# Kernel optimization log

Hardware: AMD Instinct MI355X
Metric: run time of the kernel (lower is better)

Reference implementation:

```python
import jax, jax.numpy as jnp
import numpy as np

B, M, L, H, V, HOPS = 32, 128, 32, 512, 32000, 3
NEG_INF = -1e9


def setup_inputs() -> dict:
    key = jax.random.key(0)
    k1, k2, k3, k4 = jax.random.split(key, 4)
    inputs = jax.random.randint(k1, (B, M, L), 0, V)          # memory token ids
    lengths = jax.random.randint(k2, (B, M), 1, L + 1)        # >0 so no all-masked rows
    enc_hidden = jax.random.normal(k3, (B, H), dtype=jnp.float32)
    # hop+1 embedding tables, normal_(0, 0.1) as in the torch init
    C = jax.random.normal(k4, (HOPS + 1, V, H), dtype=jnp.float32) * 0.1
    return {"inputs": inputs, "lengths": lengths, "enc_hidden": enc_hidden, "C": C}


def reference(inputs, lengths, enc_hidden, C):
    mask = lengths == 0                                       # [B, M] True -> masked

    def pool(table):
        # embedding gather [B,M,L,H] then sum over tokens -> [B,M,H]
        return table[inputs].sum(axis=2)

    u = enc_hidden                                            # [B, H]
    attns = []
    for h in range(HOPS):
        m_A = pool(C[h])                                      # [B, M, H]
        scores = jnp.einsum('bh,bmh->bm', u, m_A)             # dot attention
        scores = jnp.where(mask, NEG_INF, scores)
        attn = jax.nn.softmax(scores, axis=-1)                # [B, M]
        m_C = pool(C[h + 1])                                  # [B, M, H]
        u = u + jnp.einsum('bm,bmh->bh', attn, m_C)           # o_k combine
        attns.append(attn[:, None, :])                        # [B, 1, M] as in torch
    return u, jnp.stack(attns)                                # u_k [B,H], attns [HOPS,B,1,M]
```

## Files before the change

### kernel.cpp

```cpp
#include <hip/hip_runtime.h>

#define NB 32
#define NM 128
#define NL 32
#define NH 512
#define NV 32000
#define NHOPS 3
#define NEG_INF -1e9f

template <int NT>
__global__ __launch_bounds__(128)
void pool_kernel(const int* __restrict__ inputs,
                 const float* __restrict__ Ctab,
                 float* __restrict__ P) {
    const int bm  = blockIdx.x;
    const int tid = threadIdx.x;
    __shared__ int idx[NL];
    if (tid < NL) idx[tid] = inputs[bm * NL + tid];
    __syncthreads();

    const int hoff = tid * 4;
    float4 acc[NT];
#pragma unroll
    for (int t = 0; t < NT; ++t) acc[t] = make_float4(0.f, 0.f, 0.f, 0.f);

    for (int l = 0; l < NL; ++l) {
        const size_t rowbase = (size_t)idx[l] * NH + hoff;
#pragma unroll
        for (int t = 0; t < NT; ++t) {
            const float4 v = *reinterpret_cast<const float4*>(
                Ctab + (size_t)t * NV * NH + rowbase);
            acc[t].x += v.x; acc[t].y += v.y; acc[t].z += v.z; acc[t].w += v.w;
        }
    }
#pragma unroll
    for (int t = 0; t < NT; ++t) {
        *reinterpret_cast<float4*>(
            P + ((size_t)t * NB * NM + bm) * NH + hoff) = acc[t];
    }
}

__global__ __launch_bounds__(512)
void hop_kernel(const float* __restrict__ u_in,
                const float* __restrict__ PA,
                const float* __restrict__ PC,
                const int*   __restrict__ lengths,
                float* __restrict__ u_out,
                float* __restrict__ attn_out) {
    const int b   = blockIdx.x;
    const int tid = threadIdx.x;
    __shared__ float u_s[NH];
    __shared__ float sc[NM];
    __shared__ float tmp[512];

    u_s[tid] = u_in[b * NH + tid];
    __syncthreads();

    const int wave = tid >> 6;
    const int lane = tid & 63;
    for (int m = wave; m < NM; m += 8) {
        const float* row = PA + ((size_t)b * NM + m) * NH;
        float p = 0.f;
#pragma unroll
        for (int k = 0; k < NH / 64; ++k) {
            const int h = lane + k * 64;
            p += u_s[h] * row[h];
        }
#pragma unroll
        for (int off = 32; off; off >>= 1) p += __shfl_down(p, off, 64);
        if (lane == 0) sc[m] = p;
    }
    __syncthreads();

    float s = NEG_INF;
    if (tid < NM) s = (lengths[b * NM + tid] == 0) ? NEG_INF : sc[tid];
    tmp[tid] = s;
    __syncthreads();
    for (int st = 256; st >= 1; st >>= 1) {
        if (tid < st) tmp[tid] = fmaxf(tmp[tid], tmp[tid + st]);
        __syncthreads();
    }
    const float mx = tmp[0];
    __syncthreads();
    const float e = (tid < NM) ? expf(s - mx) : 0.f;
    tmp[tid] = e;
    __syncthreads();
    for (int st = 256; st >= 1; st >>= 1) {
        if (tid < st) tmp[tid] += tmp[tid + st];
        __syncthreads();
    }
    const float inv = 1.f / tmp[0];
    __syncthreads();
    if (tid < NM) {
        const float a = e * inv;
        sc[tid] = a;
        attn_out[b * NM + tid] = a;
    }
    __syncthreads();

    float acc = 0.f;
    for (int m = 0; m < NM; ++m) {
        acc += sc[m] * PC[((size_t)b * NM + m) * NH + tid];
    }
    u_out[b * NH + tid] = u_s[tid] + acc;
}

__global__ __launch_bounds__(128)
void scores_gather_kernel(const int* __restrict__ inputs,
                          const float* __restrict__ Ctab,
                          const float* __restrict__ u_in,
                          const int*   __restrict__ lengths,
                          float* __restrict__ scores) {
    const int bm  = blockIdx.x;
    const int b   = bm / NM;
    const int tid = threadIdx.x;
    __shared__ int idx[NL];
    if (tid < NL) idx[tid] = inputs[bm * NL + tid];
    __syncthreads();
    const int hoff = tid * 4;
    const float4 u4 = *reinterpret_cast<const float4*>(u_in + b * NH + hoff);
    float p = 0.f;
    for (int l = 0; l < NL; ++l) {
        const float4 v = *reinterpret_cast<const float4*>(
            Ctab + (size_t)idx[l] * NH + hoff);
        p += u4.x * v.x + u4.y * v.y + u4.z * v.z + u4.w * v.w;
    }
#pragma unroll
    for (int off = 32; off; off >>= 1) p += __shfl_down(p, off, 64);
    __shared__ float w2[2];
    if ((tid & 63) == 0) w2[tid >> 6] = p;
    __syncthreads();
    if (tid == 0) {
        float sres = w2[0] + w2[1];
        if (lengths[bm] == 0) sres = NEG_INF;
        scores[bm] = sres;
    }
}

__global__ __launch_bounds__(128)
void softmax_kernel(const float* __restrict__ scores,
                    float* __restrict__ attn_ws,
                    float* __restrict__ attn_out) {
    const int b   = blockIdx.x;
    const int tid = threadIdx.x;
    const float s = scores[b * NM + tid];
    float p = s;
#pragma unroll
    for (int off = 32; off; off >>= 1) p = fmaxf(p, __shfl_down(p, off, 64));
    __shared__ float w2[2];
    if ((tid & 63) == 0) w2[tid >> 6] = p;
    __syncthreads();
    const float mx = fmaxf(w2[0], w2[1]);
    const float e = expf(s - mx);
    float q = e;
#pragma unroll
    for (int off = 32; off; off >>= 1) q += __shfl_down(q, off, 64);
    __shared__ float w3[2];
    if ((tid & 63) == 0) w3[tid >> 6] = q;
    __syncthreads();
    const float a = e / (w3[0] + w3[1]);
    attn_ws[b * NM + tid]  = a;
    attn_out[b * NM + tid] = a;
}

__global__ __launch_bounds__(512)
void update_gather_kernel(const int* __restrict__ inputs,
                          const float* __restrict__ Ctab,
                          const float* __restrict__ u_in,
                          const float* __restrict__ attn,
                          float* __restrict__ u_out) {
    const int b   = blockIdx.x;
    const int tid = threadIdx.x;
    __shared__ float a_s[NM];
    __shared__ int   idx_s[NM * NL];
    if (tid < NM) a_s[tid] = attn[b * NM + tid];
    for (int i = tid; i < NM * NL; i += 512) idx_s[i] = inputs[b * NM * NL + i];
    __syncthreads();
    float acc = u_in[b * NH + tid];
    for (int m = 0; m < NM; ++m) {
        const float a = a_s[m];
        float part = 0.f;
        for (int l = 0; l < NL; ++l) {
            part += Ctab[(size_t)idx_s[m * NL + l] * NH + tid];
        }
        acc += a * part;
    }
    u_out[b * NH + tid] = acc;
}

extern "C" void kernel_launch(void* const* d_in, const int* in_sizes, int n_in,
                              void* d_out, int out_size, void* d_ws, size_t ws_size,
                              hipStream_t stream) {
    const int*   inputs  = (const int*)d_in[0];
    const int*   lengths = (const int*)d_in[1];
    const float* enc     = (const float*)d_in[2];
    const float* C       = (const float*)d_in[3];

    float* out     = (float*)d_out;
    float* u_final = out;
    float* attns   = out + NB * NH;

    const size_t POOL_ELEMS = (size_t)NB * NM * NH;
    const size_t U_ELEMS    = (size_t)NB * NH;
    float* ws = (float*)d_ws;

    if (ws_size >= (4 * POOL_ELEMS + 2 * U_ELEMS) * sizeof(float)) {
        float* P  = ws;
        float* u1 = ws + 4 * POOL_ELEMS;
        float* u2 = u1 + U_ELEMS;
        pool_kernel<4><<<NB * NM, 128, 0, stream>>>(inputs, C, P);
        const float* uin[NHOPS] = {enc, u1, u2};
        float*       uou[NHOPS] = {u1, u2, u_final};
        for (int h = 0; h < NHOPS; ++h) {
            hop_kernel<<<NB, 512, 0, stream>>>(
                uin[h], P + (size_t)h * POOL_ELEMS, P + (size_t)(h + 1) * POOL_ELEMS,
                lengths, uou[h], attns + (size_t)h * NB * NM);
        }
    } else if (ws_size >= (2 * POOL_ELEMS + 2 * U_ELEMS) * sizeof(float)) {
        float* P0 = ws;
        float* P1 = ws + POOL_ELEMS;
        float* u1 = ws + 2 * POOL_ELEMS;
        float* u2 = u1 + U_ELEMS;
        pool_kernel<2><<<NB * NM, 128, 0, stream>>>(inputs, C, P0);
        hop_kernel<<<NB, 512, 0, stream>>>(enc, P0, P1, lengths, u1, attns);
        pool_kernel<1><<<NB * NM, 128, 0, stream>>>(inputs, C + 2 * (size_t)NV * NH, P0);
        hop_kernel<<<NB, 512, 0, stream>>>(u1, P1, P0, lengths, u2, attns + NB * NM);
        pool_kernel<1><<<NB * NM, 128, 0, stream>>>(inputs, C + 3 * (size_t)NV * NH, P1);
        hop_kernel<<<NB, 512, 0, stream>>>(u2, P0, P1, lengths, u_final, attns + 2 * NB * NM);
    } else {
        float* scores  = ws;
        float* attn_ws = ws + NB * NM;
        float* u1      = attn_ws + NB * NM;
        float* u2      = u1 + U_ELEMS;
        const float* uin = enc;
        float* uou[NHOPS] = {u1, u2, u_final};
        for (int h = 0; h < NHOPS; ++h) {
            scores_gather_kernel<<<NB * NM, 128, 0, stream>>>(
                inputs, C + (size_t)h * NV * NH, uin, lengths, scores);
            softmax_kernel<<<NB, 128, 0, stream>>>(
                scores, attn_ws, attns + (size_t)h * NB * NM);
            update_gather_kernel<<<NB, 512, 0, stream>>>(
                inputs, C + (size_t)(h + 1) * NV * NH, uin, attn_ws, uou[h]);
            uin = uou[h];
        }
    }
}
```

Baseline: 206.9 us.

## Replace pooled-gather path with vocab-space GEMMs using split-bf16 MFMA scoring

Rewrites the main path algebraically. Instead of materializing pooled memories, it computes u·C[h] over the whole vocabulary as a GEMM (split-bf16 hi/lo MFMA, three products to approximate fp32), then gathers and sums the per-token scores. Attention weights are scattered into a per-batch vocabulary weight vector with atomics, so the update becomes a dense w·C[h+1] GEMM with split-K partials and a separate reduction. This replaces random row gathers over B·M·L tokens with a streaming read of each full table. The cost is a pass over the entire 32000x512 table per hop, extra kernel launches, atomic contention, and slightly reduced precision from the bf16 split.

```diff
diff --git a/kernel.cpp b/kernel.cpp
--- a/kernel.cpp
+++ b/kernel.cpp
@@ -8,111 +8,179 @@
 #define NHOPS 3
 #define NEG_INF -1e9f
 
-template <int NT>
+#define VC_D 16
+#define VC_U 128
+#define NPART (NV / VC_U)
+
+typedef __attribute__((ext_vector_type(8))) short bf16x8;
+typedef __attribute__((ext_vector_type(4))) float f32x4;
+
+__device__ __forceinline__ unsigned short f2bf(float x) {
+    unsigned u = __float_as_uint(x);
+    return (unsigned short)((u + 0x7fffu + ((u >> 16) & 1u)) >> 16);
+}
+__device__ __forceinline__ float bf2f(unsigned short h) {
+    return __uint_as_float(((unsigned)h) << 16);
+}
+
 __global__ __launch_bounds__(128)
-void pool_kernel(const int* __restrict__ inputs,
-                 const float* __restrict__ Ctab,
-                 float* __restrict__ P) {
-    const int bm  = blockIdx.x;
-    const int tid = threadIdx.x;
-    __shared__ int idx[NL];
-    if (tid < NL) idx[tid] = inputs[bm * NL + tid];
-    __syncthreads();
-
-    const int hoff = tid * 4;
-    float4 acc[NT];
-#pragma unroll
-    for (int t = 0; t < NT; ++t) acc[t] = make_float4(0.f, 0.f, 0.f, 0.f);
-
-    for (int l = 0; l < NL; ++l) {
-        const size_t rowbase = (size_t)idx[l] * NH + hoff;
-#pragma unroll
-        for (int t = 0; t < NT; ++t) {
-            const float4 v = *reinterpret_cast<const float4*>(
-                Ctab + (size_t)t * NV * NH + rowbase);
-            acc[t].x += v.x; acc[t].y += v.y; acc[t].z += v.z; acc[t].w += v.w;
-        }
-    }
-#pragma unroll
-    for (int t = 0; t < NT; ++t) {
-        *reinterpret_cast<float4*>(
-            P + ((size_t)t * NB * NM + bm) * NH + hoff) = acc[t];
-    }
-}
-
-__global__ __launch_bounds__(512)
-void hop_kernel(const float* __restrict__ u_in,
-                const float* __restrict__ PA,
-                const float* __restrict__ PC,
-                const int*   __restrict__ lengths,
-                float* __restrict__ u_out,
-                float* __restrict__ attn_out) {
-    const int b   = blockIdx.x;
-    const int tid = threadIdx.x;
-    __shared__ float u_s[NH];
-    __shared__ float sc[NM];
-    __shared__ float tmp[512];
-
-    u_s[tid] = u_in[b * NH + tid];
-    __syncthreads();
-
-    const int wave = tid >> 6;
-    const int lane = tid & 63;
-    for (int m = wave; m < NM; m += 8) {
-        const float* row = PA + ((size_t)b * NM + m) * NH;
-        float p = 0.f;
-#pragma unroll
-        for (int k = 0; k < NH / 64; ++k) {
-            const int h = lane + k * 64;
-            p += u_s[h] * row[h];
-        }
-#pragma unroll
-        for (int off = 32; off; off >>= 1) p += __shfl_down(p, off, 64);
-        if (lane == 0) sc[m] = p;
-    }
-    __syncthreads();
-
-    float s = NEG_INF;
-    if (tid < NM) s = (lengths[b * NM + tid] == 0) ? NEG_INF : sc[tid];
-    tmp[tid] = s;
-    __syncthreads();
-    for (int st = 256; st >= 1; st >>= 1) {
-        if (tid < st) tmp[tid] = fmaxf(tmp[tid], tmp[tid + st]);
-        __syncthreads();
-    }
-    const float mx = tmp[0];
-    __syncthreads();
-    const float e = (tid < NM) ? expf(s - mx) : 0.f;
-    tmp[tid] = e;
-    __syncthreads();
-    for (int st = 256; st >= 1; st >>= 1) {
-        if (tid < st) tmp[tid] += tmp[tid + st];
-        __syncthreads();
-    }
-    const float inv = 1.f / tmp[0];
-    __syncthreads();
-    if (tid < NM) {
-        const float a = e * inv;
-        sc[tid] = a;
-        attn_out[b * NM + tid] = a;
-    }
-    __syncthreads();
-
-    float acc = 0.f;
-    for (int m = 0; m < NM; ++m) {
-        acc += sc[m] * PC[((size_t)b * NM + m) * NH + tid];
-    }
-    u_out[b * NH + tid] = u_s[tid] + acc;
+void gemm_D_kernel(const float* __restrict__ u,
+                   const float* __restrict__ Ct,
+                   float* __restrict__ D) {
+    __shared__ __align__(16) unsigned short Ch[VC_D * NH];
+    __shared__ __align__(16) unsigned short Cl[VC_D * NH];
+    const int tid = threadIdx.x;
+    const int vbase = blockIdx.x * VC_D;
+
+#pragma unroll
+    for (int k = 0; k < 16; ++k) {
+        const int v = k;
+        const int c4 = tid;
+        float4 x = *reinterpret_cast<const float4*>(
+            Ct + ((size_t)(vbase + v) << 9) + (c4 << 2));
+        unsigned short h0 = f2bf(x.x), h1 = f2bf(x.y), h2 = f2bf(x.z), h3 = f2bf(x.w);
+        unsigned short l0 = f2bf(x.x - bf2f(h0)), l1 = f2bf(x.y - bf2f(h1)),
+                       l2 = f2bf(x.z - bf2f(h2)), l3 = f2bf(x.w - bf2f(h3));
+        int us = ((v << 9) + (c4 << 2)) ^ ((v & 7) << 3);
+        *reinterpret_cast<ushort4*>(&Ch[us]) = make_ushort4(h0, h1, h2, h3);
+        *reinterpret_cast<ushort4*>(&Cl[us]) = make_ushort4(l0, l1, l2, l3);
+    }
+    __syncthreads();
+
+    const int wave = tid >> 6, lane = tid & 63;
+    const int mt = wave;
+    const int arow = mt * 16 + (lane & 15);
+    const int kblk = (lane >> 4) * 8;
+    const int brow = lane & 15;
+    f32x4 acc = {0.f, 0.f, 0.f, 0.f};
+
+    for (int kt = 0; kt < 16; ++kt) {
+        const int koff = kt * 32 + kblk;
+        const float* up = u + (arow << 9) + koff;
+        float4 a0 = *reinterpret_cast<const float4*>(up);
+        float4 a1 = *reinterpret_cast<const float4*>(up + 4);
+        float av[8] = {a0.x, a0.y, a0.z, a0.w, a1.x, a1.y, a1.z, a1.w};
+        bf16x8 ah, al;
+#pragma unroll
+        for (int j = 0; j < 8; ++j) {
+            unsigned short h = f2bf(av[j]);
+            ah[j] = (short)h;
+            al[j] = (short)f2bf(av[j] - bf2f(h));
+        }
+        const int rb = ((brow << 9) + koff) ^ ((brow & 7) << 3);
+        bf16x8 bh = *reinterpret_cast<const bf16x8*>(&Ch[rb]);
+        bf16x8 bl = *reinterpret_cast<const bf16x8*>(&Cl[rb]);
+        acc = __builtin_amdgcn_mfma_f32_16x16x32_bf16(ah, bh, acc, 0, 0, 0);
+        acc = __builtin_amdgcn_mfma_f32_16x16x32_bf16(ah, bl, acc, 0, 0, 0);
+        acc = __builtin_amdgcn_mfma_f32_16x16x32_bf16(al, bh, acc, 0, 0, 0);
+    }
+    const int vcol = vbase + (lane & 15);
+    const int b0 = mt * 16 + (lane >> 4) * 4;
+#pragma unroll
+    for (int r = 0; r < 4; ++r)
+        D[(size_t)(b0 + r) * NV + vcol] = acc[r];
+}
+
+__global__ __launch_bounds__(128)
+void scores_kernel(const float* __restrict__ D,
+                   const int* __restrict__ inputs,
+                   const int* __restrict__ lengths,
+                   float* __restrict__ attn_out,
+                   float* __restrict__ w) {
+    const int b = blockIdx.x, m = threadIdx.x;
+    const float* Db = D + (size_t)b * NV;
+    int idx[NL];
+    const int4* ip = reinterpret_cast<const int4*>(inputs + (((b << 7) + m) << 5));
+#pragma unroll
+    for (int q = 0; q < 8; ++q) {
+        int4 i4 = ip[q];
+        idx[q * 4 + 0] = i4.x; idx[q * 4 + 1] = i4.y;
+        idx[q * 4 + 2] = i4.z; idx[q * 4 + 3] = i4.w;
+    }
+    float s = 0.f;
+#pragma unroll
+    for (int l = 0; l < NL; ++l) s += Db[idx[l]];
+    if (lengths[(b << 7) + m] == 0) s = NEG_INF;
+
+    const int lane = m & 63, wv = m >> 6;
+    __shared__ float red[2];
+    float mx = s;
+#pragma unroll
+    for (int o = 32; o; o >>= 1) mx = fmaxf(mx, __shfl_xor(mx, o, 64));
+    if (lane == 0) red[wv] = mx;
+    __syncthreads();
+    mx = fmaxf(red[0], red[1]);
+    const float e = expf(s - mx);
+    __syncthreads();
+    float sum = e;
+#pragma unroll
+    for (int o = 32; o; o >>= 1) sum += __shfl_xor(sum, o, 64);
+    if (lane == 0) red[wv] = sum;
+    __syncthreads();
+    const float a = e / (red[0] + red[1]);
+    attn_out[(b << 7) + m] = a;
+
+    float* wb = w + (size_t)b * NV;
+    for (int i = m; i < NV; i += 128) wb[i] = 0.f;
+    __syncthreads();
+#pragma unroll
+    for (int l = 0; l < NL; ++l) atomicAdd(&wb[idx[l]], a);
+}
+
+__global__ __launch_bounds__(256)
+void gemm_U_kernel(const float* __restrict__ w,
+                   const float* __restrict__ Ct,
+                   float* __restrict__ part) {
+    __shared__ float wsm[NB][VC_U];
+    const int tid = threadIdx.x;
+    const int vbase = blockIdx.x * VC_U;
+#pragma unroll
+    for (int k = 0; k < 16; ++k) {
+        int i = k * 256 + tid;
+        int b = i >> 7, v = i & 127;
+        wsm[b][v] = w[(size_t)b * NV + vbase + v];
+    }
+    __syncthreads();
+    const int h0 = tid << 1;
+    float2 acc[NB];
+#pragma unroll
+    for (int b = 0; b < NB; ++b) acc[b] = make_float2(0.f, 0.f);
+
+    for (int v = 0; v < VC_U; v += 2) {
+        float2 c0 = *reinterpret_cast<const float2*>(Ct + ((size_t)(vbase + v) << 9) + h0);
+        float2 c1 = *reinterpret_cast<const float2*>(Ct + ((size_t)(vbase + v + 1) << 9) + h0);
+#pragma unroll
+        for (int b = 0; b < NB; ++b) {
+            float2 wv = *reinterpret_cast<const float2*>(&wsm[b][v]);
+            acc[b].x += wv.x * c0.x + wv.y * c1.x;
+            acc[b].y += wv.x * c0.y + wv.y * c1.y;
+        }
+    }
+    float* pb = part + (size_t)blockIdx.x * NB * NH;
+#pragma unroll
+    for (int b = 0; b < NB; ++b)
+        *reinterpret_cast<float2*>(pb + (b << 9) + h0) = acc[b];
+}
+
+__global__ __launch_bounds__(256)
+void reduce_u_kernel(const float* __restrict__ u_in,
+                     const float* __restrict__ part,
+                     float* __restrict__ u_out) {
+    const int e = blockIdx.x * 256 + threadIdx.x;
+    float a = u_in[e];
+#pragma unroll 10
+    for (int p = 0; p < NPART; ++p) a += part[(size_t)p * (NB * NH) + e];
+    u_out[e] = a;
 }
 
 __global__ __launch_bounds__(128)
 void scores_gather_kernel(const int* __restrict__ inputs,
                           const float* __restrict__ Ctab,
                           const float* __restrict__ u_in,
-                          const int*   __restrict__ lengths,
+                          const int* __restrict__ lengths,
                           float* __restrict__ scores) {
-    const int bm  = blockIdx.x;
-    const int b   = bm / NM;
+    const int bm = blockIdx.x;
+    const int b = bm / NM;
     const int tid = threadIdx.x;
     __shared__ int idx[NL];
     if (tid < NL) idx[tid] = inputs[bm * NL + tid];
@@ -141,7 +209,7 @@
 void softmax_kernel(const float* __restrict__ scores,
                     float* __restrict__ attn_ws,
                     float* __restrict__ attn_out) {
-    const int b   = blockIdx.x;
+    const int b = blockIdx.x;
     const int tid = threadIdx.x;
     const float s = scores[b * NM + tid];
     float p = s;
@@ -159,7 +227,7 @@
     if ((tid & 63) == 0) w3[tid >> 6] = q;
     __syncthreads();
     const float a = e / (w3[0] + w3[1]);
-    attn_ws[b * NM + tid]  = a;
+    attn_ws[b * NM + tid] = a;
     attn_out[b * NM + tid] = a;
 }
 
@@ -169,10 +237,10 @@
                           const float* __restrict__ u_in,
                           const float* __restrict__ attn,
                           float* __restrict__ u_out) {
-    const int b   = blockIdx.x;
+    const int b = blockIdx.x;
     const int tid = threadIdx.x;
     __shared__ float a_s[NM];
-    __shared__ int   idx_s[NM * NL];
+    __shared__ int idx_s[NM * NL];
     if (tid < NM) a_s[tid] = attn[b * NM + tid];
     for (int i = tid; i < NM * NL; i += 512) idx_s[i] = inputs[b * NM * NL + i];
     __syncthreads();
@@ -200,33 +268,29 @@
     float* u_final = out;
     float* attns   = out + NB * NH;
 
-    const size_t POOL_ELEMS = (size_t)NB * NM * NH;
-    const size_t U_ELEMS    = (size_t)NB * NH;
+    const size_t TAB = (size_t)NV * NH;
+    const size_t BV  = (size_t)NB * NV;
+    const size_t U_ELEMS = (size_t)NB * NH;
     float* ws = (float*)d_ws;
 
-    if (ws_size >= (4 * POOL_ELEMS + 2 * U_ELEMS) * sizeof(float)) {
-        float* P  = ws;
-        float* u1 = ws + 4 * POOL_ELEMS;
-        float* u2 = u1 + U_ELEMS;
-        pool_kernel<4><<<NB * NM, 128, 0, stream>>>(inputs, C, P);
-        const float* uin[NHOPS] = {enc, u1, u2};
-        float*       uou[NHOPS] = {u1, u2, u_final};
+    const size_t need = (2 * BV + 2 * U_ELEMS + (size_t)NPART * U_ELEMS) * sizeof(float);
+
+    if (ws_size >= need) {
+        float* D    = ws;
+        float* w    = D + BV;
+        float* u1   = w + BV;
+        float* u2   = u1 + U_ELEMS;
+        float* part = u2 + U_ELEMS;
+
+        const float* uin[NHOPS]  = {enc, u1, u2};
+        float*       unext[NHOPS] = {u1, u2, u_final};
         for (int h = 0; h < NHOPS; ++h) {
-            hop_kernel<<<NB, 512, 0, stream>>>(
-                uin[h], P + (size_t)h * POOL_ELEMS, P + (size_t)(h + 1) * POOL_ELEMS,
-                lengths, uou[h], attns + (size_t)h * NB * NM);
-        }
-    } else if (ws_size >= (2 * POOL_ELEMS + 2 * U_ELEMS) * sizeof(float)) {
-        float* P0 = ws;
-        float* P1 = ws + POOL_ELEMS;
-        float* u1 = ws + 2 * POOL_ELEMS;
-        float* u2 = u1 + U_ELEMS;
-        pool_kernel<2><<<NB * NM, 128, 0, stream>>>(inputs, C, P0);
-        hop_kernel<<<NB, 512, 0, stream>>>(enc, P0, P1, lengths, u1, attns);
-        pool_kernel<1><<<NB * NM, 128, 0, stream>>>(inputs, C + 2 * (size_t)NV * NH, P0);
-        hop_kernel<<<NB, 512, 0, stream>>>(u1, P1, P0, lengths, u2, attns + NB * NM);
-        pool_kernel<1><<<NB * NM, 128, 0, stream>>>(inputs, C + 3 * (size_t)NV * NH, P1);
-        hop_kernel<<<NB, 512, 0, stream>>>(u2, P0, P1, lengths, u_final, attns + 2 * NB * NM);
+            gemm_D_kernel<<<NV / VC_D, 128, 0, stream>>>(uin[h], C + (size_t)h * TAB, D);
+            scores_kernel<<<NB, 128, 0, stream>>>(D, inputs, lengths,
+                                                  attns + (size_t)h * NB * NM, w);
+            gemm_U_kernel<<<NPART, 256, 0, stream>>>(w, C + (size_t)(h + 1) * TAB, part);
+            reduce_u_kernel<<<(NB * NH) / 256, 256, 0, stream>>>(uin[h], part, unext[h]);
+        }
     } else {
         float* scores  = ws;
         float* attn_ws = ws + NB * NM;
@@ -236,11 +300,11 @@
         float* uou[NHOPS] = {u1, u2, u_final};
         for (int h = 0; h < NHOPS; ++h) {
             scores_gather_kernel<<<NB * NM, 128, 0, stream>>>(
-                inputs, C + (size_t)h * NV * NH, uin, lengths, scores);
+                inputs, C + (size_t)h * TAB, uin, lengths, scores);
             softmax_kernel<<<NB, 128, 0, stream>>>(
                 scores, attn_ws, attns + (size_t)h * NB * NM);
             update_gather_kernel<<<NB, 512, 0, stream>>>(
-                inputs, C + (size_t)(h + 1) * NV * NH, uin, attn_ws, uou[h]);
+                inputs, C + (size_t)(h + 1) * TAB, uin, attn_ws, uou[h]);
             uin = uou[h];
         }
     }
```

Result: slower. 416.8 us (+101.4%).
